# Kernel tuning notes

Hardware: AMD Instinct MI355X
Metric: run time of the kernel (lower is better)

## Reference

```python
import jax, jax.numpy as jnp
import numpy as np

B, S, DIM = 2, 2048, 1024
H, W = 16, 256
HD = DIM // H
SCALE = HD ** -0.5


def setup_inputs() -> dict:
    key = jax.random.key(0)
    ks = jax.random.split(key, 9)
    std = DIM ** -0.5
    return {
        "x": jax.random.normal(ks[0], (B, S, DIM), dtype=jnp.float32),
        "Wq": jax.random.normal(ks[1], (DIM, DIM), dtype=jnp.float32) * std,
        "bq": jnp.zeros((DIM,), dtype=jnp.float32),
        "Wk": jax.random.normal(ks[2], (DIM, DIM), dtype=jnp.float32) * std,
        "bk": jnp.zeros((DIM,), dtype=jnp.float32),
        "Wv": jax.random.normal(ks[3], (DIM, DIM), dtype=jnp.float32) * std,
        "bv": jnp.zeros((DIM,), dtype=jnp.float32),
        "Wo": jax.random.normal(ks[4], (DIM, DIM), dtype=jnp.float32) * std,
        "bo": jnp.zeros((DIM,), dtype=jnp.float32),
    }


def reference(x, Wq, bq, Wk, bk, Wv, bv, Wo, bo):
    b, s, dim = x.shape
    q = (x @ Wq + bq).reshape(b, s, H, HD).transpose(0, 2, 1, 3)  # [B,H,S,HD]
    k = (x @ Wk + bk).reshape(b, s, H, HD).transpose(0, 2, 1, 3)
    v = (x @ Wv + bv).reshape(b, s, H, HD).transpose(0, 2, 1, 3)

    scores = jnp.einsum("bhid,bhjd->bhij", q, k) * SCALE  # [B,H,S,S]
    i = jnp.arange(s)[:, None]
    j = jnp.arange(s)[None, :]
    # valid keys: within causal sliding window [i-W+1, i]
    valid = (j <= i) & (j >= i - W + 1)
    scores = jnp.where(valid, scores, -jnp.inf)
    attn = jax.nn.softmax(scores, axis=-1)
    out = jnp.einsum("bhij,bhjd->bhid", attn, v)  # [B,H,S,HD]
    out = out.transpose(0, 2, 1, 3).reshape(b, s, dim)
    return out @ Wo + bo
```

## Files before the change

kernel.cpp:

```cpp
#include <hip/hip_runtime.h>
#include <stdint.h>

typedef __bf16 bf16;
typedef __bf16 bf16x8 __attribute__((ext_vector_type(8)));
typedef float f32x4 __attribute__((ext_vector_type(4)));

#define MFMA16(a, b, c) __builtin_amdgcn_mfma_f32_16x16x32_bf16((a), (b), (c), 0, 0, 0)

__device__ __forceinline__ void ldsdma16(const void* g, void* l) {
  __builtin_amdgcn_global_load_lds((const __attribute__((address_space(1))) void*)g,
                                   (__attribute__((address_space(3))) void*)l, 16, 0, 0);
}

__global__ __launch_bounds__(256) void prep_kernel(const float* __restrict__ x,
                                                   const float* __restrict__ Wq,
                                                   const float* __restrict__ Wk,
                                                   const float* __restrict__ Wv,
                                                   const float* __restrict__ Wo,
                                                   bf16* __restrict__ WT,
                                                   bf16* __restrict__ xb) {
  if (blockIdx.z == 4) {
    const int t = (blockIdx.y * 16 + blockIdx.x) * 256 + threadIdx.x;
#pragma unroll
    for (int it = 0; it < 16; ++it) {
      const int idx = (it * 65536 + t) * 4;
      float4 v = *(const float4*)(x + idx);
      union { bf16 h[4]; uint2 u; } p;
      p.h[0] = (bf16)v.x; p.h[1] = (bf16)v.y; p.h[2] = (bf16)v.z; p.h[3] = (bf16)v.w;
      *(uint2*)(xb + idx) = p.u;
    }
    return;
  }
  __shared__ float tile[64][65];
  const float* src = blockIdx.z == 0 ? Wq : blockIdx.z == 1 ? Wk : blockIdx.z == 2 ? Wv : Wo;
  bf16* dst = WT + (size_t)blockIdx.z * 1024 * 1024;
  const int k0 = blockIdx.y * 64, n0 = blockIdx.x * 64;
  const int rr = threadIdx.x >> 6, c = threadIdx.x & 63;
#pragma unroll
  for (int i = 0; i < 16; ++i) {
    int r = i * 4 + rr;
    tile[r][c] = src[(size_t)(k0 + r) * 1024 + n0 + c];
  }
  __syncthreads();
#pragma unroll
  for (int i = 0; i < 16; ++i) {
    int r = i * 4 + rr;
    dst[(size_t)(n0 + r) * 1024 + k0 + c] = (bf16)tile[c][r];
  }
}

__global__ __launch_bounds__(256) void qkv_gemm(const bf16* __restrict__ xb,
                                                const bf16* __restrict__ WT,
                                                const float* __restrict__ bq,
                                                const float* __restrict__ bk,
                                                const float* __restrict__ bv,
                                                bf16* __restrict__ QKVc) {
  __shared__ bf16 As[128 * 64] __attribute__((aligned(16)));
  __shared__ bf16 Bs[128 * 64] __attribute__((aligned(16)));
  const int tid = threadIdx.x, lane = tid & 63, wave = tid >> 6;
  const int wm = wave >> 1, wn = wave & 1;
  const int quad = lane >> 4, l16 = lane & 15;
  const int m0 = blockIdx.y * 128, n0 = blockIdx.x * 128;

  f32x4 acc[4][4];
  const f32x4 zero = {0.f, 0.f, 0.f, 0.f};
#pragma unroll
  for (int i = 0; i < 4; ++i)
#pragma unroll
    for (int j = 0; j < 4; ++j) acc[i][j] = zero;

  for (int k0 = 0; k0 < 1024; k0 += 64) {
#pragma unroll
    for (int b2 = 0; b2 < 4; ++b2) {
      int chunk = wave * 256 + b2 * 64 + lane;
      int row = chunk >> 3;
      int cg = (chunk & 7) ^ (row & 7);
      ldsdma16(xb + (size_t)(m0 + row) * 1024 + k0 + cg * 8,
               (char*)As + (size_t)(wave * 256 + b2 * 64) * 16);
      ldsdma16(WT + (size_t)(n0 + row) * 1024 + k0 + cg * 8,
               (char*)Bs + (size_t)(wave * 256 + b2 * 64) * 16);
    }
    __syncthreads();
#pragma unroll
    for (int s = 0; s < 2; ++s) {
      bf16x8 af[4], bfv[4];
#pragma unroll
      for (int i = 0; i < 4; ++i) {
        int ra = wm * 64 + i * 16 + l16;
        af[i] = ((const bf16x8*)As)[ra * 8 + ((s * 4 + quad) ^ (ra & 7))];
        int rb = wn * 64 + i * 16 + l16;
        bfv[i] = ((const bf16x8*)Bs)[rb * 8 + ((s * 4 + quad) ^ (rb & 7))];
      }
#pragma unroll
      for (int i = 0; i < 4; ++i)
#pragma unroll
        for (int j = 0; j < 4; ++j) acc[i][j] = MFMA16(af[i], bfv[j], acc[i][j]);
    }
    __syncthreads();
  }

  const int sel = blockIdx.x >> 3;
  const float* bp = sel == 0 ? bq : sel == 1 ? bk : bv;
  const float scl = (sel == 0) ? 0.18033688f : 1.f;
#pragma unroll
  for (int j = 0; j < 4; ++j) {
    const int n = n0 + wn * 64 + j * 16 + l16;
    const float bias = bp[n & 1023];
#pragma unroll
    for (int i = 0; i < 4; ++i) {
#pragma unroll
      for (int r = 0; r < 4; ++r) {
        const int token = m0 + wm * 64 + i * 16 + quad * 4 + r;
        QKVc[(size_t)token * 3072 + n] = (bf16)((acc[i][j][r] + bias) * scl);
      }
    }
  }
}

__global__ __launch_bounds__(256) void v_transpose(const bf16* __restrict__ QKVc,
                                                   bf16* __restrict__ Vt) {
  __shared__ bf16 tile[64][72] __attribute__((aligned(16)));
  const int tid = threadIdx.x;
  const int st = blockIdx.x, h = blockIdx.y, b = blockIdx.z;
  {
    const int t = tid >> 2, cg = (tid & 3) * 16;
    const bf16* src = QKVc + ((size_t)(b * 2048 + st * 64 + t)) * 3072 + 2048 + h * 64 + cg;
    bf16x8 v0 = *(const bf16x8*)src;
    bf16x8 v1 = *(const bf16x8*)(src + 8);
    *(bf16x8*)&tile[t][cg] = v0;
    *(bf16x8*)&tile[t][cg + 8] = v1;
  }
  __syncthreads();
  const int hd = tid & 63, sg = (tid >> 6) * 16;
  bf16 o[16];
#pragma unroll
  for (int i = 0; i < 16; ++i) o[i] = tile[sg + i][hd];
  bf16* dst = Vt + ((size_t)((b * 16 + h) * 64 + hd)) * 2048 + st * 64 + sg;
  *(bf16x8*)dst = *(bf16x8*)&o[0];
  *(bf16x8*)(dst + 8) = *(bf16x8*)&o[8];
}

__global__ __launch_bounds__(256) void attn_kernel(const bf16* __restrict__ QKVc,
                                                   const bf16* __restrict__ Vt,
                                                   bf16* __restrict__ Ao) {
  __shared__ bf16 Ps[4][16 * 72] __attribute__((aligned(16)));

  const int tid = threadIdx.x, lane = tid & 63, wave = tid >> 6;
  const int quad = lane >> 4, l16 = lane & 15;
  const int qt = blockIdx.x, h = blockIdx.y, b = blockIdx.z;
  const int q0 = qt * 64;
  const bf16* Vb = Vt + ((size_t)(b * 16 + h)) * 2048 * 64;

  const int qrow = wave * 16 + l16;
  const bf16* qp = QKVc + (size_t)(b * 2048 + q0 + qrow) * 3072 + h * 64 + quad * 8;
  const bf16x8 qa0 = *(const bf16x8*)qp;
  const bf16x8 qa1 = *(const bf16x8*)(qp + 32);

  float lrow[4];
  f32x4 oacc[4];
  const f32x4 zero = {0.f, 0.f, 0.f, 0.f};
#pragma unroll
  for (int r = 0; r < 4; ++r) lrow[r] = 0.f;
#pragma unroll
  for (int t = 0; t < 4; ++t) oacc[t] = zero;

  const int clo = (qt >= 4) ? (qt - 4) : 0;
  for (int ck = clo; ck <= qt; ++ck) {
    const int c0 = ck * 64;

    f32x4 sc[4];
#pragma unroll
    for (int nt = 0; nt < 4; ++nt) {
      const bf16* kp = QKVc + (size_t)(b * 2048 + c0 + nt * 16 + l16) * 3072 + 1024 + h * 64 + quad * 8;
      bf16x8 kb0 = *(const bf16x8*)kp;
      bf16x8 kb1 = *(const bf16x8*)(kp + 32);
      f32x4 s = MFMA16(qa0, kb0, zero);
      sc[nt] = MFMA16(qa1, kb1, s);
    }

    bf16x8 vb0[4], vb1[4];
#pragma unroll
    for (int ht = 0; ht < 4; ++ht) {
      const bf16* vp = Vb + (size_t)(ht * 16 + l16) * 2048 + c0 + quad * 8;
      vb0[ht] = *(const bf16x8*)vp;
      vb1[ht] = *(const bf16x8*)(vp + 32);
    }

    if (ck == qt) {
#pragma unroll
      for (int r = 0; r < 4; ++r) {
        const int i = q0 + wave * 16 + quad * 4 + r;
#pragma unroll
        for (int nt = 0; nt < 4; ++nt) {
          const int j = c0 + nt * 16 + l16;
          const float p = (j <= i) ? exp2f(sc[nt][r]) : 0.f;
          sc[nt][r] = p;
          lrow[r] += p;
        }
      }
    } else if (qt >= 4 && ck == qt - 4) {
#pragma unroll
      for (int r = 0; r < 4; ++r) {
        const int i = q0 + wave * 16 + quad * 4 + r;
#pragma unroll
        for (int nt = 0; nt < 4; ++nt) {
          const int j = c0 + nt * 16 + l16;
          const float p = (j + 255 >= i) ? exp2f(sc[nt][r]) : 0.f;
          sc[nt][r] = p;
          lrow[r] += p;
        }
      }
    } else {
#pragma unroll
      for (int r = 0; r < 4; ++r) {
#pragma unroll
        for (int nt = 0; nt < 4; ++nt) {
          const float p = exp2f(sc[nt][r]);
          sc[nt][r] = p;
          lrow[r] += p;
        }
      }
    }

#pragma unroll
    for (int nt = 0; nt < 4; ++nt)
#pragma unroll
      for (int r = 0; r < 4; ++r)
        Ps[wave][(quad * 4 + r) * 72 + nt * 16 + l16] = (bf16)sc[nt][r];
    asm volatile("s_waitcnt lgkmcnt(0)" ::: "memory");
    bf16x8 pa0 = ((const bf16x8*)Ps[wave])[l16 * 9 + quad];
    bf16x8 pa1 = ((const bf16x8*)Ps[wave])[l16 * 9 + 4 + quad];

#pragma unroll
    for (int ht = 0; ht < 4; ++ht) {
      f32x4 o = MFMA16(pa0, vb0[ht], oacc[ht]);
      oacc[ht] = MFMA16(pa1, vb1[ht], o);
    }
  }

#pragma unroll
  for (int r = 0; r < 4; ++r) {
#pragma unroll
    for (int m = 8; m >= 1; m >>= 1) lrow[r] += __shfl_xor(lrow[r], m, 64);
    const float inv = 1.f / lrow[r];
    const int row = q0 + wave * 16 + quad * 4 + r;
    const size_t outb = ((size_t)(b * 2048 + row)) * 1024 + h * 64;
#pragma unroll
    for (int ht = 0; ht < 4; ++ht)
      Ao[outb + ht * 16 + l16] = (bf16)(oacc[ht][r] * inv);
  }
}

__global__ __launch_bounds__(256) void out_gemm(const bf16* __restrict__ Ain,
                                                const bf16* __restrict__ WoT,
                                                const float* __restrict__ bo,
                                                float* __restrict__ out) {
  __shared__ bf16 As[128 * 64] __attribute__((aligned(16)));
  __shared__ bf16 Bs[64 * 64] __attribute__((aligned(16)));
  const int tid = threadIdx.x, lane = tid & 63, wave = tid >> 6;
  const int wm = wave >> 1, wn = wave & 1;
  const int quad = lane >> 4, l16 = lane & 15;
  const int m0 = blockIdx.y * 128, n0 = blockIdx.x * 64;

  f32x4 acc[4][2];
  const f32x4 zero = {0.f, 0.f, 0.f, 0.f};
#pragma unroll
  for (int i = 0; i < 4; ++i)
#pragma unroll
    for (int j = 0; j < 2; ++j) acc[i][j] = zero;

  for (int k0 = 0; k0 < 1024; k0 += 64) {
#pragma unroll
    for (int b2 = 0; b2 < 4; ++b2) {
      int chunk = wave * 256 + b2 * 64 + lane;
      int row = chunk >> 3;
      int cg = (chunk & 7) ^ (row & 7);
      ldsdma16(Ain + (size_t)(m0 + row) * 1024 + k0 + cg * 8,
               (char*)As + (size_t)(wave * 256 + b2 * 64) * 16);
    }
#pragma unroll
    for (int b2 = 0; b2 < 2; ++b2) {
      int chunk = wave * 128 + b2 * 64 + lane;
      int row = chunk >> 3;
      int cg = (chunk & 7) ^ (row & 7);
      ldsdma16(WoT + (size_t)(n0 + row) * 1024 + k0 + cg * 8,
               (char*)Bs + (size_t)(wave * 128 + b2 * 64) * 16);
    }
    __syncthreads();
#pragma unroll
    for (int s = 0; s < 2; ++s) {
      bf16x8 af[4], bfv[2];
#pragma unroll
      for (int i = 0; i < 4; ++i) {
        int ra = wm * 64 + i * 16 + l16;
        af[i] = ((const bf16x8*)As)[ra * 8 + ((s * 4 + quad) ^ (ra & 7))];
      }
#pragma unroll
      for (int j = 0; j < 2; ++j) {
        int rb = wn * 32 + j * 16 + l16;
        bfv[j] = ((const bf16x8*)Bs)[rb * 8 + ((s * 4 + quad) ^ (rb & 7))];
      }
#pragma unroll
      for (int i = 0; i < 4; ++i)
#pragma unroll
        for (int j = 0; j < 2; ++j) acc[i][j] = MFMA16(af[i], bfv[j], acc[i][j]);
    }
    __syncthreads();
  }

#pragma unroll
  for (int j = 0; j < 2; ++j) {
    const int n = n0 + wn * 32 + j * 16 + l16;
    const float bias = bo[n];
#pragma unroll
    for (int i = 0; i < 4; ++i) {
#pragma unroll
      for (int r = 0; r < 4; ++r) {
        const int token = m0 + wm * 64 + i * 16 + quad * 4 + r;
        out[(size_t)token * 1024 + n] = acc[i][j][r] + bias;
      }
    }
  }
}

extern "C" void kernel_launch(void* const* d_in, const int* in_sizes, int n_in,
                              void* d_out, int out_size, void* d_ws, size_t ws_size,
                              hipStream_t stream) {
  const float* x  = (const float*)d_in[0];
  const float* Wq = (const float*)d_in[1];
  const float* bq = (const float*)d_in[2];
  const float* Wk = (const float*)d_in[3];
  const float* bk = (const float*)d_in[4];
  const float* Wv = (const float*)d_in[5];
  const float* bv = (const float*)d_in[6];
  const float* Wo = (const float*)d_in[7];
  const float* bo = (const float*)d_in[8];
  float* out = (float*)d_out;

  char* ws = (char*)d_ws;
  bf16* xb   = (bf16*)(ws);
  bf16* WT   = (bf16*)(ws + ((size_t)8 << 20));
  bf16* QKVc = (bf16*)(ws + ((size_t)16 << 20));
  bf16* Vt   = (bf16*)(ws + ((size_t)40 << 20));
  bf16* Ao   = (bf16*)(ws + ((size_t)48 << 20));

  prep_kernel<<<dim3(16, 16, 5), 256, 0, stream>>>(x, Wq, Wk, Wv, Wo, WT, xb);
  qkv_gemm<<<dim3(24, 32), 256, 0, stream>>>(xb, WT, bq, bk, bv, QKVc);
  v_transpose<<<dim3(32, 16, 2), 256, 0, stream>>>(QKVc, Vt);
  attn_kernel<<<dim3(32, 16, 2), 256, 0, stream>>>(QKVc, Vt, Ao);
  out_gemm<<<dim3(16, 32), 256, 0, stream>>>(Ao, WT + (size_t)3 * 1024 * 1024, bo, out);
}
```

Measured before the change: 193.3 us.

## Load A operand directly from global into registers, stage only B in LDS with K=128

Both the QKV and output GEMMs stop staging the activation (A) tile in shared memory. Each lane now reads its MFMA A fragment straight from global memory, while only the weight tile is staged in LDS with a wider K-step of 128 per barrier. This halves the number of sync phases and the LDS traffic. The output GEMM tile is also reshaped from 128x64 to 64x128, with a matching grid. The risk is uncoalesced, latency-exposed global loads for A that the compiler can no longer hide behind the LDS-DMA.

```diff
diff --git a/kernel.cpp b/kernel.cpp
--- a/kernel.cpp
+++ b/kernel.cpp
@@ -55,8 +55,7 @@
                                                 const float* __restrict__ bk,
                                                 const float* __restrict__ bv,
                                                 bf16* __restrict__ QKVc) {
-  __shared__ bf16 As[128 * 64] __attribute__((aligned(16)));
-  __shared__ bf16 Bs[128 * 64] __attribute__((aligned(16)));
+  __shared__ bf16 Bs[128 * 128] __attribute__((aligned(16)));
   const int tid = threadIdx.x, lane = tid & 63, wave = tid >> 6;
   const int wm = wave >> 1, wn = wave & 1;
   const int quad = lane >> 4, l16 = lane & 15;
@@ -69,27 +68,32 @@
 #pragma unroll
     for (int j = 0; j < 4; ++j) acc[i][j] = zero;
 
-  for (int k0 = 0; k0 < 1024; k0 += 64) {
-#pragma unroll
-    for (int b2 = 0; b2 < 4; ++b2) {
-      int chunk = wave * 256 + b2 * 64 + lane;
-      int row = chunk >> 3;
-      int cg = (chunk & 7) ^ (row & 7);
-      ldsdma16(xb + (size_t)(m0 + row) * 1024 + k0 + cg * 8,
-               (char*)As + (size_t)(wave * 256 + b2 * 64) * 16);
-      ldsdma16(WT + (size_t)(n0 + row) * 1024 + k0 + cg * 8,
-               (char*)Bs + (size_t)(wave * 256 + b2 * 64) * 16);
+  const bf16* Arow[4];
+#pragma unroll
+  for (int i = 0; i < 4; ++i)
+    Arow[i] = xb + (size_t)(m0 + wm * 64 + i * 16 + l16) * 1024 + quad * 8;
+
+  for (int ph = 0; ph < 8; ++ph) {
+    const int kp = ph * 128;
+#pragma unroll
+    for (int inst = 0; inst < 8; ++inst) {
+      int d = inst * 256 + wave * 64 + lane;
+      int row = d >> 4, dc = d & 15;
+      int sc = (dc & 8) | ((dc & 7) ^ (row & 7));
+      ldsdma16(WT + (size_t)(n0 + row) * 1024 + kp + sc * 8,
+               (char*)Bs + (size_t)(inst * 256 + wave * 64) * 16);
     }
     __syncthreads();
 #pragma unroll
-    for (int s = 0; s < 2; ++s) {
+    for (int s = 0; s < 4; ++s) {
       bf16x8 af[4], bfv[4];
 #pragma unroll
       for (int i = 0; i < 4; ++i) {
-        int ra = wm * 64 + i * 16 + l16;
-        af[i] = ((const bf16x8*)As)[ra * 8 + ((s * 4 + quad) ^ (ra & 7))];
+        af[i] = *(const bf16x8*)(Arow[i] + kp + s * 32);
         int rb = wn * 64 + i * 16 + l16;
-        bfv[i] = ((const bf16x8*)Bs)[rb * 8 + ((s * 4 + quad) ^ (rb & 7))];
+        int c = s * 4 + quad;
+        int dc = (c & 8) | ((c & 7) ^ (rb & 7));
+        bfv[i] = ((const bf16x8*)Bs)[rb * 16 + dc];
       }
 #pragma unroll
       for (int i = 0; i < 4; ++i)
@@ -255,68 +259,64 @@
                                                 const bf16* __restrict__ WoT,
                                                 const float* __restrict__ bo,
                                                 float* __restrict__ out) {
-  __shared__ bf16 As[128 * 64] __attribute__((aligned(16)));
-  __shared__ bf16 Bs[64 * 64] __attribute__((aligned(16)));
+  __shared__ bf16 Bs[128 * 128] __attribute__((aligned(16)));
   const int tid = threadIdx.x, lane = tid & 63, wave = tid >> 6;
   const int wm = wave >> 1, wn = wave & 1;
   const int quad = lane >> 4, l16 = lane & 15;
-  const int m0 = blockIdx.y * 128, n0 = blockIdx.x * 64;
-
-  f32x4 acc[4][2];
+  const int m0 = blockIdx.y * 64, n0 = blockIdx.x * 128;
+
+  f32x4 acc[2][4];
   const f32x4 zero = {0.f, 0.f, 0.f, 0.f};
 #pragma unroll
-  for (int i = 0; i < 4; ++i)
-#pragma unroll
-    for (int j = 0; j < 2; ++j) acc[i][j] = zero;
-
-  for (int k0 = 0; k0 < 1024; k0 += 64) {
-#pragma unroll
-    for (int b2 = 0; b2 < 4; ++b2) {
-      int chunk = wave * 256 + b2 * 64 + lane;
-      int row = chunk >> 3;
-      int cg = (chunk & 7) ^ (row & 7);
-      ldsdma16(Ain + (size_t)(m0 + row) * 1024 + k0 + cg * 8,
-               (char*)As + (size_t)(wave * 256 + b2 * 64) * 16);
-    }
-#pragma unroll
-    for (int b2 = 0; b2 < 2; ++b2) {
-      int chunk = wave * 128 + b2 * 64 + lane;
-      int row = chunk >> 3;
-      int cg = (chunk & 7) ^ (row & 7);
-      ldsdma16(WoT + (size_t)(n0 + row) * 1024 + k0 + cg * 8,
-               (char*)Bs + (size_t)(wave * 128 + b2 * 64) * 16);
+  for (int i = 0; i < 2; ++i)
+#pragma unroll
+    for (int j = 0; j < 4; ++j) acc[i][j] = zero;
+
+  const bf16* Arow[2];
+#pragma unroll
+  for (int i = 0; i < 2; ++i)
+    Arow[i] = Ain + (size_t)(m0 + wm * 32 + i * 16 + l16) * 1024 + quad * 8;
+
+  for (int ph = 0; ph < 8; ++ph) {
+    const int kp = ph * 128;
+#pragma unroll
+    for (int inst = 0; inst < 8; ++inst) {
+      int d = inst * 256 + wave * 64 + lane;
+      int row = d >> 4, dc = d & 15;
+      int sc = (dc & 8) | ((dc & 7) ^ (row & 7));
+      ldsdma16(WoT + (size_t)(n0 + row) * 1024 + kp + sc * 8,
+               (char*)Bs + (size_t)(inst * 256 + wave * 64) * 16);
     }
     __syncthreads();
 #pragma unroll
-    for (int s = 0; s < 2; ++s) {
-      bf16x8 af[4], bfv[2];
-#pragma unroll
-      for (int i = 0; i < 4; ++i) {
-        int ra = wm * 64 + i * 16 + l16;
-        af[i] = ((const bf16x8*)As)[ra * 8 + ((s * 4 + quad) ^ (ra & 7))];
-      }
-#pragma unroll
-      for (int j = 0; j < 2; ++j) {
-        int rb = wn * 32 + j * 16 + l16;
-        bfv[j] = ((const bf16x8*)Bs)[rb * 8 + ((s * 4 + quad) ^ (rb & 7))];
-      }
-#pragma unroll
-      for (int i = 0; i < 4; ++i)
-#pragma unroll
-        for (int j = 0; j < 2; ++j) acc[i][j] = MFMA16(af[i], bfv[j], acc[i][j]);
+    for (int s = 0; s < 4; ++s) {
+      bf16x8 af[2], bfv[4];
+#pragma unroll
+      for (int i = 0; i < 2; ++i) af[i] = *(const bf16x8*)(Arow[i] + kp + s * 32);
+#pragma unroll
+      for (int j = 0; j < 4; ++j) {
+        int rb = wn * 64 + j * 16 + l16;
+        int c = s * 4 + quad;
+        int dc = (c & 8) | ((c & 7) ^ (rb & 7));
+        bfv[j] = ((const bf16x8*)Bs)[rb * 16 + dc];
+      }
+#pragma unroll
+      for (int i = 0; i < 2; ++i)
+#pragma unroll
+        for (int j = 0; j < 4; ++j) acc[i][j] = MFMA16(af[i], bfv[j], acc[i][j]);
     }
     __syncthreads();
   }
 
 #pragma unroll
-  for (int j = 0; j < 2; ++j) {
-    const int n = n0 + wn * 32 + j * 16 + l16;
+  for (int j = 0; j < 4; ++j) {
+    const int n = n0 + wn * 64 + j * 16 + l16;
     const float bias = bo[n];
 #pragma unroll
-    for (int i = 0; i < 4; ++i) {
-#pragma unroll
-      for (int r = 0; r < 4; ++r) {
-        const int token = m0 + wm * 64 + i * 16 + quad * 4 + r;
+    for (int i = 0; i < 2; ++i) {
+#pragma unroll
+      for (int r = 0; r < 4; ++r) {
+        const int token = m0 + wm * 32 + i * 16 + quad * 4 + r;
         out[(size_t)token * 1024 + n] = acc[i][j][r] + bias;
       }
     }
@@ -348,5 +348,5 @@
   qkv_gemm<<<dim3(24, 32), 256, 0, stream>>>(xb, WT, bq, bk, bv, QKVc);
   v_transpose<<<dim3(32, 16, 2), 256, 0, stream>>>(QKVc, Vt);
   attn_kernel<<<dim3(32, 16, 2), 256, 0, stream>>>(QKVc, Vt, Ao);
-  out_gemm<<<dim3(16, 32), 256, 0, stream>>>(Ao, WT + (size_t)3 * 1024 * 1024, bo, out);
-}
+  out_gemm<<<dim3(8, 64), 256, 0, stream>>>(Ao, WT + (size_t)3 * 1024 * 1024, bo, out);
+}
```

New measurement: 235.9 us. 1.22x slower.

## Stage Q/K/V tiles in LDS with double-buffered DMA and 128-row query blocks

Applied to the files above, without the earlier changes.

The attention kernel now processes 128 query rows per block, with each wave handling two 16-row tiles. Q is loaded into LDS once, and K/V chunks are double-buffered in LDS using async global_load_lds with an XOR swizzle, so each K/V load is shared by more query rows. This replaces per-wave direct global loads of K and V. The cost is more LDS, half as many blocks (which may lower occupancy and parallelism), and a slightly wider key range per block.

```diff
diff --git a/kernel.cpp b/kernel.cpp
--- a/kernel.cpp
+++ b/kernel.cpp
@@ -141,113 +141,157 @@
 }
 
 __global__ __launch_bounds__(256) void attn_kernel(const bf16* __restrict__ QKVc,
-                                                   const bf16* __restrict__ Vt,
+                                                   const bf16* __restrict__ VtG,
                                                    bf16* __restrict__ Ao) {
-  __shared__ bf16 Ps[4][16 * 72] __attribute__((aligned(16)));
+  __shared__ bf16 Qs[128 * 64] __attribute__((aligned(16)));
+  __shared__ bf16 Ks[2][64 * 64] __attribute__((aligned(16)));
+  __shared__ bf16 Vs[2][64 * 64] __attribute__((aligned(16)));
+  __shared__ bf16 Ps[4][2][16 * 72] __attribute__((aligned(16)));
 
   const int tid = threadIdx.x, lane = tid & 63, wave = tid >> 6;
   const int quad = lane >> 4, l16 = lane & 15;
   const int qt = blockIdx.x, h = blockIdx.y, b = blockIdx.z;
-  const int q0 = qt * 64;
-  const bf16* Vb = Vt + ((size_t)(b * 16 + h)) * 2048 * 64;
-
-  const int qrow = wave * 16 + l16;
-  const bf16* qp = QKVc + (size_t)(b * 2048 + q0 + qrow) * 3072 + h * 64 + quad * 8;
-  const bf16x8 qa0 = *(const bf16x8*)qp;
-  const bf16x8 qa1 = *(const bf16x8*)(qp + 32);
-
-  float lrow[4];
-  f32x4 oacc[4];
+  const int q0 = qt * 128;
+  const size_t vbase = (size_t)(b * 16 + h) * 131072;
+
+#pragma unroll
+  for (int inst = 0; inst < 4; ++inst) {
+    int d = inst * 256 + wave * 64 + lane;
+    int row = d >> 3, cc = d & 7;
+    ldsdma16(QKVc + (size_t)(b * 2048 + q0 + row) * 3072 + h * 64 + ((cc ^ (row & 7)) * 8),
+             (char*)Qs + (size_t)(inst * 256 + wave * 64) * 16);
+  }
+
+  const int lo = (qt >= 2) ? (2 * qt - 4) : 0;
+  const int hi = 2 * qt + 1;
+
+  auto stage_kv = [&](int ck, int bu) {
+    const int c0k = ck * 64;
+#pragma unroll
+    for (int inst = 0; inst < 2; ++inst) {
+      int d = inst * 256 + wave * 64 + lane;
+      int row = d >> 3, cc = d & 7;
+      int sc = (cc ^ (row & 7)) * 8;
+      ldsdma16(QKVc + (size_t)(b * 2048 + c0k + row) * 3072 + 1024 + h * 64 + sc,
+               (char*)Ks[bu] + (size_t)(inst * 256 + wave * 64) * 16);
+      ldsdma16(VtG + vbase + (size_t)row * 2048 + c0k + sc,
+               (char*)Vs[bu] + (size_t)(inst * 256 + wave * 64) * 16);
+    }
+  };
+
+  stage_kv(lo, lo & 1);
+  __syncthreads();
+
+  bf16x8 qa[2][2];
+#pragma unroll
+  for (int rt = 0; rt < 2; ++rt) {
+    int row = wave * 32 + rt * 16 + l16;
+#pragma unroll
+    for (int s = 0; s < 2; ++s)
+      qa[rt][s] = ((const bf16x8*)Qs)[row * 8 + ((s * 4 + quad) ^ (row & 7))];
+  }
+
+  float lrow[2][4];
+  f32x4 oacc[2][4];
   const f32x4 zero = {0.f, 0.f, 0.f, 0.f};
 #pragma unroll
-  for (int r = 0; r < 4; ++r) lrow[r] = 0.f;
-#pragma unroll
-  for (int t = 0; t < 4; ++t) oacc[t] = zero;
-
-  const int clo = (qt >= 4) ? (qt - 4) : 0;
-  for (int ck = clo; ck <= qt; ++ck) {
+  for (int rt = 0; rt < 2; ++rt)
+#pragma unroll
+    for (int r = 0; r < 4; ++r) { lrow[rt][r] = 0.f; oacc[rt][r] = zero; }
+
+  for (int ck = lo; ck <= hi; ++ck) {
+    if (ck > lo) __syncthreads();
+    if (ck < hi) stage_kv(ck + 1, (ck + 1) & 1);
+    const int bu = ck & 1;
     const int c0 = ck * 64;
 
-    f32x4 sc[4];
+    bf16x8 kb[4][2], vb[4][2];
 #pragma unroll
     for (int nt = 0; nt < 4; ++nt) {
-      const bf16* kp = QKVc + (size_t)(b * 2048 + c0 + nt * 16 + l16) * 3072 + 1024 + h * 64 + quad * 8;
-      bf16x8 kb0 = *(const bf16x8*)kp;
-      bf16x8 kb1 = *(const bf16x8*)(kp + 32);
-      f32x4 s = MFMA16(qa0, kb0, zero);
-      sc[nt] = MFMA16(qa1, kb1, s);
-    }
-
-    bf16x8 vb0[4], vb1[4];
-#pragma unroll
-    for (int ht = 0; ht < 4; ++ht) {
-      const bf16* vp = Vb + (size_t)(ht * 16 + l16) * 2048 + c0 + quad * 8;
-      vb0[ht] = *(const bf16x8*)vp;
-      vb1[ht] = *(const bf16x8*)(vp + 32);
-    }
-
-    if (ck == qt) {
-#pragma unroll
-      for (int r = 0; r < 4; ++r) {
-        const int i = q0 + wave * 16 + quad * 4 + r;
-#pragma unroll
-        for (int nt = 0; nt < 4; ++nt) {
-          const int j = c0 + nt * 16 + l16;
-          const float p = (j <= i) ? exp2f(sc[nt][r]) : 0.f;
-          sc[nt][r] = p;
-          lrow[r] += p;
+      int rr = nt * 16 + l16;
+#pragma unroll
+      for (int s = 0; s < 2; ++s) {
+        kb[nt][s] = ((const bf16x8*)Ks[bu])[rr * 8 + ((s * 4 + quad) ^ (rr & 7))];
+        vb[nt][s] = ((const bf16x8*)Vs[bu])[rr * 8 + ((s * 4 + quad) ^ (rr & 7))];
+      }
+    }
+
+#pragma unroll
+    for (int rt = 0; rt < 2; ++rt) {
+      f32x4 sc4[4];
+#pragma unroll
+      for (int nt = 0; nt < 4; ++nt) {
+        f32x4 s = MFMA16(qa[rt][0], kb[nt][0], zero);
+        sc4[nt] = MFMA16(qa[rt][1], kb[nt][1], s);
+      }
+
+      if (ck >= 2 * qt) {
+#pragma unroll
+        for (int r = 0; r < 4; ++r) {
+          const int i = q0 + wave * 32 + rt * 16 + quad * 4 + r;
+#pragma unroll
+          for (int nt = 0; nt < 4; ++nt) {
+            const int j = c0 + nt * 16 + l16;
+            const float p = (j <= i) ? exp2f(sc4[nt][r]) : 0.f;
+            sc4[nt][r] = p;
+            lrow[rt][r] += p;
+          }
         }
-      }
-    } else if (qt >= 4 && ck == qt - 4) {
-#pragma unroll
-      for (int r = 0; r < 4; ++r) {
-        const int i = q0 + wave * 16 + quad * 4 + r;
-#pragma unroll
-        for (int nt = 0; nt < 4; ++nt) {
-          const int j = c0 + nt * 16 + l16;
-          const float p = (j + 255 >= i) ? exp2f(sc[nt][r]) : 0.f;
-          sc[nt][r] = p;
-          lrow[r] += p;
+      } else if (ck <= 2 * qt - 3) {
+#pragma unroll
+        for (int r = 0; r < 4; ++r) {
+          const int i = q0 + wave * 32 + rt * 16 + quad * 4 + r;
+#pragma unroll
+          for (int nt = 0; nt < 4; ++nt) {
+            const int j = c0 + nt * 16 + l16;
+            const float p = (j + 255 >= i) ? exp2f(sc4[nt][r]) : 0.f;
+            sc4[nt][r] = p;
+            lrow[rt][r] += p;
+          }
         }
-      }
-    } else {
-#pragma unroll
-      for (int r = 0; r < 4; ++r) {
-#pragma unroll
-        for (int nt = 0; nt < 4; ++nt) {
-          const float p = exp2f(sc[nt][r]);
-          sc[nt][r] = p;
-          lrow[r] += p;
+      } else {
+#pragma unroll
+        for (int r = 0; r < 4; ++r) {
+#pragma unroll
+          for (int nt = 0; nt < 4; ++nt) {
+            const float p = exp2f(sc4[nt][r]);
+            sc4[nt][r] = p;
+            lrow[rt][r] += p;
+          }
         }
       }
-    }
-
-#pragma unroll
-    for (int nt = 0; nt < 4; ++nt)
-#pragma unroll
-      for (int r = 0; r < 4; ++r)
-        Ps[wave][(quad * 4 + r) * 72 + nt * 16 + l16] = (bf16)sc[nt][r];
-    asm volatile("s_waitcnt lgkmcnt(0)" ::: "memory");
-    bf16x8 pa0 = ((const bf16x8*)Ps[wave])[l16 * 9 + quad];
-    bf16x8 pa1 = ((const bf16x8*)Ps[wave])[l16 * 9 + 4 + quad];
-
-#pragma unroll
-    for (int ht = 0; ht < 4; ++ht) {
-      f32x4 o = MFMA16(pa0, vb0[ht], oacc[ht]);
-      oacc[ht] = MFMA16(pa1, vb1[ht], o);
-    }
-  }
-
-#pragma unroll
-  for (int r = 0; r < 4; ++r) {
-#pragma unroll
-    for (int m = 8; m >= 1; m >>= 1) lrow[r] += __shfl_xor(lrow[r], m, 64);
-    const float inv = 1.f / lrow[r];
-    const int row = q0 + wave * 16 + quad * 4 + r;
-    const size_t outb = ((size_t)(b * 2048 + row)) * 1024 + h * 64;
-#pragma unroll
-    for (int ht = 0; ht < 4; ++ht)
-      Ao[outb + ht * 16 + l16] = (bf16)(oacc[ht][r] * inv);
+
+#pragma unroll
+      for (int nt = 0; nt < 4; ++nt)
+#pragma unroll
+        for (int r = 0; r < 4; ++r)
+          Ps[wave][rt][(quad * 4 + r) * 72 + nt * 16 + l16] = (bf16)sc4[nt][r];
+      asm volatile("s_waitcnt lgkmcnt(0)" ::: "memory");
+      bf16x8 pa0 = ((const bf16x8*)Ps[wave][rt])[l16 * 9 + quad];
+      bf16x8 pa1 = ((const bf16x8*)Ps[wave][rt])[l16 * 9 + 4 + quad];
+
+#pragma unroll
+      for (int ht = 0; ht < 4; ++ht) {
+        f32x4 o = MFMA16(pa0, vb[ht][0], oacc[rt][ht]);
+        oacc[rt][ht] = MFMA16(pa1, vb[ht][1], o);
+      }
+    }
+  }
+
+#pragma unroll
+  for (int rt = 0; rt < 2; ++rt) {
+#pragma unroll
+    for (int r = 0; r < 4; ++r) {
+      float lr = lrow[rt][r];
+#pragma unroll
+      for (int m = 8; m >= 1; m >>= 1) lr += __shfl_xor(lr, m, 64);
+      const float inv = 1.f / lr;
+      const int row = q0 + wave * 32 + rt * 16 + quad * 4 + r;
+      const size_t outb = ((size_t)(b * 2048 + row)) * 1024 + h * 64;
+#pragma unroll
+      for (int ht = 0; ht < 4; ++ht)
+        Ao[outb + ht * 16 + l16] = (bf16)(oacc[rt][ht][r] * inv);
+    }
   }
 }
 
@@ -347,6 +391,6 @@
   prep_kernel<<<dim3(16, 16, 5), 256, 0, stream>>>(x, Wq, Wk, Wv, Wo, WT, xb);
   qkv_gemm<<<dim3(24, 32), 256, 0, stream>>>(xb, WT, bq, bk, bv, QKVc);
   v_transpose<<<dim3(32, 16, 2), 256, 0, stream>>>(QKVc, Vt);
-  attn_kernel<<<dim3(32, 16, 2), 256, 0, stream>>>(QKVc, Vt, Ao);
+  attn_kernel<<<dim3(16, 16, 2), 256, 0, stream>>>(QKVc, Vt, Ao);
   out_gemm<<<dim3(16, 32), 256, 0, stream>>>(Ao, WT + (size_t)3 * 1024 * 1024, bo, out);
 }
```

Result: faster. 176.1 us (-8.9%).
